# Kernel tuning notes

Hardware: AMD Instinct MI355X
Metric: run time of the kernel (lower is better)

The kernel has to match this reference:

```python
import jax, jax.numpy as jnp
import numpy as np
from jax import lax

BN_EPS = 1e-5

def _maxpool_same(x, k):
    # x: [B, C, H, W]; stride-1 max pool with 'same' padding (pad value -inf, like torch)
    p = k // 2
    neg_inf = jnp.array(-jnp.inf, dtype=x.dtype)
    return lax.reduce_window(x, neg_inf, lax.max,
                             window_dimensions=(1, 1, k, k),
                             window_strides=(1, 1, 1, 1),
                             padding=[(0, 0), (0, 0), (p, p), (p, p)])

def setup_inputs() -> dict:
    key = jax.random.key(0)
    k1, k2 = jax.random.split(key)
    B, Cin, Cout, H, W_ = 16, 1024, 512, 32, 32
    x = jax.random.normal(k1, (B, Cin, H, W_), dtype=jnp.float32)
    W = jax.random.normal(k2, (Cout, Cin), dtype=jnp.float32) * (1.0 / np.sqrt(Cin))
    gamma = jnp.ones((Cout,), dtype=jnp.float32)
    beta = jnp.zeros((Cout,), dtype=jnp.float32)
    running_mean = jnp.zeros((Cout,), dtype=jnp.float32)
    running_var = jnp.ones((Cout,), dtype=jnp.float32)
    return {"x": x, "W": W, "gamma": gamma, "beta": beta,
            "running_mean": running_mean, "running_var": running_var}

def reference(x, W, gamma, beta, running_mean, running_var):
    # 1x1 conv (no bias): [B, Cin, H, W] x [Cout, Cin] -> [B, Cout, H, W]
    y = jnp.einsum('bchw,oc->bohw', x, W)
    # BatchNorm (inference form with running stats)
    inv = gamma * lax.rsqrt(running_var + BN_EPS)
    y = y * inv[None, :, None, None] + (beta - running_mean * inv)[None, :, None, None]
    # Mish activation
    y = y * jnp.tanh(jax.nn.softplus(y))
    # Three overlapping stride-1 max pools, concat channel-wise: [m13, m9, m5, y]
    return jnp.concatenate([_maxpool_same(y, 13), _maxpool_same(y, 9),
                            _maxpool_same(y, 5), y], axis=1)
```

## Files before the change

### kernel.cpp

```cpp
#include <hip/hip_runtime.h>
#include <hip/hip_bf16.h>
#include <math.h>

typedef __attribute__((ext_vector_type(4))) float  f32x4;
typedef __attribute__((ext_vector_type(8))) __bf16 bf16x8;
typedef __attribute__((ext_vector_type(4))) __bf16 bf16x4;

#define BN_EPS 1e-5f

__device__ __forceinline__ void gload16(const void* g, void* l) {
    __builtin_amdgcn_global_load_lds(
        (const __attribute__((address_space(1))) unsigned int*)g,
        (__attribute__((address_space(3))) unsigned int*)l, 16, 0, 0);
}

__global__ __launch_bounds__(256) void prep_transpose_kernel(
    const float* __restrict__ x, __bf16* __restrict__ xt,
    const float* __restrict__ W, const float* __restrict__ gamma,
    const float* __restrict__ beta, const float* __restrict__ rmean,
    const float* __restrict__ rvar, __bf16* __restrict__ Wb,
    float* __restrict__ sc, float* __restrict__ bs)
{
    __shared__ float lt[64][65];
    const int t = threadIdx.x;
    const int bid = blockIdx.x;

    if (bid >= 4096) {
        const int b2 = bid - 4096;
        const int t2 = b2 * 256 + t;
        const int idx = t2 * 4;
        f32x4 v = *(const f32x4*)(W + idx);
        bf16x4 o;
        o[0] = (__bf16)v[0]; o[1] = (__bf16)v[1];
        o[2] = (__bf16)v[2]; o[3] = (__bf16)v[3];
        *(bf16x4*)(Wb + idx) = o;
        if (b2 < 2) {
            int ch = b2 * 256 + t;
            float s = gamma[ch] * rsqrtf(rvar[ch] + BN_EPS);
            sc[ch] = s;
            bs[ch] = beta[ch] - rmean[ch] * s;
        }
        return;
    }

    const int b = bid >> 8;
    const int w = bid & 255;
    const int c0  = (w & 15) * 64;
    const int hw0 = (w >> 4) * 64;

    const int cl = t >> 4;
    const int q  = (t & 15) * 4;
    const float* src = x + (((size_t)(b * 1024 + c0 + cl)) << 10) + hw0 + q;
    #pragma unroll
    for (int i = 0; i < 4; ++i) {
        f32x4 v = *(const f32x4*)(src + ((size_t)i << 14));
        int c = cl + i * 16;
        lt[c][q + 0] = v[0]; lt[c][q + 1] = v[1];
        lt[c][q + 2] = v[2]; lt[c][q + 3] = v[3];
    }
    __syncthreads();

    const int hwl = t >> 3;
    const int oct = (t & 7) * 8;
    #pragma unroll
    for (int half = 0; half < 2; ++half) {
        const int hw = hwl + half * 32;
        bf16x8 v;
        #pragma unroll
        for (int i = 0; i < 8; ++i)
            v[i] = (__bf16)lt[oct + i][hw];
        *(bf16x8*)(xt + (((size_t)(b * 1024 + hw0 + hw)) << 10) + c0 + oct) = v;
    }
}

__global__ __launch_bounds__(256, 4) void gemm_kernel(
    const __bf16* __restrict__ Wb,
    const __bf16* __restrict__ xt,
    const float* __restrict__ sc, const float* __restrict__ bs,
    float* __restrict__ out)
{
    __shared__ __align__(16) char lds[32768];
    char* const Alds = lds;
    char* const Blds = lds + 16384;

    const int t  = threadIdx.x;
    const int f  = blockIdx.x + 4 * (blockIdx.y + 8 * blockIdx.z);
    const int f2 = (f & 7) * 64 + (f >> 3);
    const int o0  = (f2 & 3) * 128;
    const int hw0 = ((f2 >> 2) & 7) * 128;
    const int b   = f2 >> 5;

    const int srow = t >> 3;
    const int sswz = ((t & 7) ^ ((t >> 3) & 7)) * 16;
    const char* Ag = (const char*)Wb + (((size_t)(o0 + srow)) << 11) + sswz;
    const char* Bg = (const char*)xt + ((size_t)b << 21)
                   + (((size_t)(hw0 + srow)) << 11) + sswz;
    char* Al = Alds + t * 16;
    char* Bl = Blds + t * 16;

    const int l  = t & 63;
    const int lr = l & 15;
    const int lk = l >> 4;
    const int wm = (t >> 6) & 1;
    const int wn = t >> 7;

    int aoff[4][2], boff[4][2];
    #pragma unroll
    for (int i = 0; i < 4; ++i)
        #pragma unroll
        for (int kk = 0; kk < 2; ++kk) {
            int ra = wm * 64 + i * 16 + lr;
            int rb = wn * 64 + i * 16 + lr;
            int s  = lk + kk * 4;
            aoff[i][kk] = ra * 128 + ((s ^ (ra & 7)) * 16);
            boff[i][kk] = rb * 128 + ((s ^ (rb & 7)) * 16);
        }

    f32x4 acc[4][4] = {};

    for (int ks = 0; ks < 16; ++ks) {
        __syncthreads();
        const int kb = ks * 128;
        #pragma unroll
        for (int i = 0; i < 4; ++i) {
            gload16(Ag + (i << 16) + kb, Al + (i << 12));
            gload16(Bg + (i << 16) + kb, Bl + (i << 12));
        }
        __syncthreads();
        #pragma unroll
        for (int kk = 0; kk < 2; ++kk) {
            bf16x8 af[4], bfr[4];
            #pragma unroll
            for (int i = 0; i < 4; ++i)
                af[i]  = *(const bf16x8*)(Alds + aoff[i][kk]);
            #pragma unroll
            for (int j = 0; j < 4; ++j)
                bfr[j] = *(const bf16x8*)(Blds + boff[j][kk]);
            #pragma unroll
            for (int i = 0; i < 4; ++i)
                #pragma unroll
                for (int j = 0; j < 4; ++j)
                    acc[i][j] = __builtin_amdgcn_mfma_f32_16x16x32_bf16(
                        af[i], bfr[j], acc[i][j], 0, 0, 0);
        }
    }

    const size_t outbase = (((size_t)b * 2048 + 1536) << 10);
    #pragma unroll
    for (int i = 0; i < 4; ++i) {
        const int ob = o0 + wm * 64 + i * 16 + lk * 4;
        const f32x4 s4 = *(const f32x4*)(sc + ob);
        const f32x4 b4 = *(const f32x4*)(bs + ob);
        #pragma unroll
        for (int r = 0; r < 4; ++r) {
            float* orow = out + outbase + (((size_t)(ob + r)) << 10)
                        + hw0 + wn * 64 + lr;
            #pragma unroll
            for (int j = 0; j < 4; ++j) {
                float v = acc[i][j][r] * s4[r] + b4[r];
                float e   = __expf(fminf(v, 15.0f));
                float num = e * (e + 2.0f);
                orow[j * 16] = v * (num / (num + 2.0f));
            }
        }
    }
}

__global__ __launch_bounds__(256) void pool_kernel(float* __restrict__ out)
{
    __shared__ float A[32][33];
    __shared__ float B[32][33];
    const int t  = threadIdx.x;
    const int id = blockIdx.x;
    const int x8 = id & 7;
    const int j  = id >> 3;
    const int b  = 2 * x8 + (j >> 8);
    const int o2 = (j & 255) * 2;
    const int r  = t >> 3;
    const int c0 = (t & 7) * 4;

    for (int ci = 0; ci < 2; ++ci) {
        const int o = o2 + ci;
        const size_t ybase = ((size_t)(b * 2048 + 1536 + o)) << 10;
        f32x4 v = *(const f32x4*)(out + ybase + t * 4);
        A[r][c0] = v[0]; A[r][c0 + 1] = v[1]; A[r][c0 + 2] = v[2]; A[r][c0 + 3] = v[3];
        __syncthreads();

        for (int p = 0; p < 3; ++p) {
            float wv[8];
            #pragma unroll
            for (int k = 0; k < 8; ++k) {
                int cc = c0 - 2 + k;
                wv[k] = (cc >= 0 && cc < 32) ? A[r][cc] : -INFINITY;
            }
            #pragma unroll
            for (int q = 0; q < 4; ++q) {
                float h = fmaxf(fmaxf(fmaxf(wv[q], wv[q + 1]), fmaxf(wv[q + 2], wv[q + 3])), wv[q + 4]);
                B[r][c0 + q] = h;
            }
            __syncthreads();
            f32x4 m;
            m[0] = m[1] = m[2] = m[3] = -INFINITY;
            #pragma unroll
            for (int k = 0; k < 5; ++k) {
                int rr = r - 2 + k;
                if (rr >= 0 && rr < 32) {
                    m[0] = fmaxf(m[0], B[rr][c0]);
                    m[1] = fmaxf(m[1], B[rr][c0 + 1]);
                    m[2] = fmaxf(m[2], B[rr][c0 + 2]);
                    m[3] = fmaxf(m[3], B[rr][c0 + 3]);
                }
            }
            A[r][c0] = m[0]; A[r][c0 + 1] = m[1]; A[r][c0 + 2] = m[2]; A[r][c0 + 3] = m[3];
            const size_t obase = ((size_t)(b * 2048 + (2 - p) * 512 + o)) << 10;
            *(f32x4*)(out + obase + t * 4) = m;
            __syncthreads();
        }
    }
}

extern "C" void kernel_launch(void* const* d_in, const int* in_sizes, int n_in,
                              void* d_out, int out_size, void* d_ws, size_t ws_size,
                              hipStream_t stream)
{
    const float* x     = (const float*)d_in[0];
    const float* W     = (const float*)d_in[1];
    const float* gamma = (const float*)d_in[2];
    const float* beta  = (const float*)d_in[3];
    const float* rmean = (const float*)d_in[4];
    const float* rvar  = (const float*)d_in[5];
    float* out = (float*)d_out;
    char*  ws  = (char*)d_ws;

    __bf16* xt = (__bf16*)ws;
    __bf16* Wb = (__bf16*)(ws + 33554432);
    float*  sc = (float*)(ws + 34603008);
    float*  bs = (float*)(ws + 34605056);

    prep_transpose_kernel<<<4608, 256, 0, stream>>>(x, xt, W, gamma, beta, rmean, rvar, Wb, sc, bs);
    gemm_kernel<<<dim3(4, 8, 16), 256, 0, stream>>>(Wb, xt, sc, bs, out);
    pool_kernel<<<4096, 256, 0, stream>>>(out);
}
```

Before: 68.65 us.

## Fuse x transpose and bf16 cast into GEMM B-tile loading

Removes the separate transpose kernel that wrote x as a bf16 channel-last copy into workspace. The GEMM now streams fp32 x tiles straight into a larger, swizzled LDS buffer and converts to bf16 while assembling MFMA B fragments. This drops a full read-write pass over the 64MB input. In exchange it doubles LDS bytes per B tile, lowers occupancy to 3 blocks, does scalar LDS reads with conversions in the inner loop, and rereads fp32 x across the 4 output-channel blocks.

```diff
diff --git a/kernel.cpp b/kernel.cpp
--- a/kernel.cpp
+++ b/kernel.cpp
@@ -14,72 +14,33 @@
         (__attribute__((address_space(3))) unsigned int*)l, 16, 0, 0);
 }
 
-__global__ __launch_bounds__(256) void prep_transpose_kernel(
-    const float* __restrict__ x, __bf16* __restrict__ xt,
+__global__ __launch_bounds__(256) void prep_kernel(
     const float* __restrict__ W, const float* __restrict__ gamma,
     const float* __restrict__ beta, const float* __restrict__ rmean,
     const float* __restrict__ rvar, __bf16* __restrict__ Wb,
     float* __restrict__ sc, float* __restrict__ bs)
 {
-    __shared__ float lt[64][65];
-    const int t = threadIdx.x;
-    const int bid = blockIdx.x;
-
-    if (bid >= 4096) {
-        const int b2 = bid - 4096;
-        const int t2 = b2 * 256 + t;
-        const int idx = t2 * 4;
-        f32x4 v = *(const f32x4*)(W + idx);
-        bf16x4 o;
-        o[0] = (__bf16)v[0]; o[1] = (__bf16)v[1];
-        o[2] = (__bf16)v[2]; o[3] = (__bf16)v[3];
-        *(bf16x4*)(Wb + idx) = o;
-        if (b2 < 2) {
-            int ch = b2 * 256 + t;
-            float s = gamma[ch] * rsqrtf(rvar[ch] + BN_EPS);
-            sc[ch] = s;
-            bs[ch] = beta[ch] - rmean[ch] * s;
-        }
-        return;
-    }
-
-    const int b = bid >> 8;
-    const int w = bid & 255;
-    const int c0  = (w & 15) * 64;
-    const int hw0 = (w >> 4) * 64;
-
-    const int cl = t >> 4;
-    const int q  = (t & 15) * 4;
-    const float* src = x + (((size_t)(b * 1024 + c0 + cl)) << 10) + hw0 + q;
-    #pragma unroll
-    for (int i = 0; i < 4; ++i) {
-        f32x4 v = *(const f32x4*)(src + ((size_t)i << 14));
-        int c = cl + i * 16;
-        lt[c][q + 0] = v[0]; lt[c][q + 1] = v[1];
-        lt[c][q + 2] = v[2]; lt[c][q + 3] = v[3];
-    }
-    __syncthreads();
-
-    const int hwl = t >> 3;
-    const int oct = (t & 7) * 8;
-    #pragma unroll
-    for (int half = 0; half < 2; ++half) {
-        const int hw = hwl + half * 32;
-        bf16x8 v;
-        #pragma unroll
-        for (int i = 0; i < 8; ++i)
-            v[i] = (__bf16)lt[oct + i][hw];
-        *(bf16x8*)(xt + (((size_t)(b * 1024 + hw0 + hw)) << 10) + c0 + oct) = v;
-    }
-}
-
-__global__ __launch_bounds__(256, 4) void gemm_kernel(
+    int t = blockIdx.x * 256 + threadIdx.x;
+    int idx = t * 4;
+    f32x4 v = *(const f32x4*)(W + idx);
+    bf16x4 o;
+    o[0] = (__bf16)v[0]; o[1] = (__bf16)v[1];
+    o[2] = (__bf16)v[2]; o[3] = (__bf16)v[3];
+    *(bf16x4*)(Wb + idx) = o;
+    if (t < 512) {
+        float s = gamma[t] * rsqrtf(rvar[t] + BN_EPS);
+        sc[t] = s;
+        bs[t] = beta[t] - rmean[t] * s;
+    }
+}
+
+__global__ __launch_bounds__(256, 3) void gemm_kernel(
     const __bf16* __restrict__ Wb,
-    const __bf16* __restrict__ xt,
+    const float* __restrict__ x,
     const float* __restrict__ sc, const float* __restrict__ bs,
     float* __restrict__ out)
 {
-    __shared__ __align__(16) char lds[32768];
+    __shared__ __align__(16) char lds[49152];
     char* const Alds = lds;
     char* const Blds = lds + 16384;
 
@@ -93,10 +54,18 @@
     const int srow = t >> 3;
     const int sswz = ((t & 7) ^ ((t >> 3) & 7)) * 16;
     const char* Ag = (const char*)Wb + (((size_t)(o0 + srow)) << 11) + sswz;
-    const char* Bg = (const char*)xt + ((size_t)b << 21)
-                   + (((size_t)(hw0 + srow)) << 11) + sswz;
     char* Al = Alds + t * 16;
+
+    int srcoff[8];
+    #pragma unroll
+    for (int r = 0; r < 8; ++r) {
+        int g = r * 256 + t;
+        int c = g >> 5, sp = g & 31;
+        int s = sp ^ (((c >> 3) & 3) << 2);
+        srcoff[r] = c * 1024 + s * 4;
+    }
     char* Bl = Blds + t * 16;
+    const float* xb = x + ((size_t)b << 20) + hw0;
 
     const int l  = t & 63;
     const int lr = l & 15;
@@ -104,17 +73,21 @@
     const int wm = (t >> 6) & 1;
     const int wn = t >> 7;
 
-    int aoff[4][2], boff[4][2];
+    int aoff[4][2];
     #pragma unroll
     for (int i = 0; i < 4; ++i)
         #pragma unroll
         for (int kk = 0; kk < 2; ++kk) {
             int ra = wm * 64 + i * 16 + lr;
-            int rb = wn * 64 + i * 16 + lr;
             int s  = lk + kk * 4;
             aoff[i][kk] = ra * 128 + ((s ^ (ra & 7)) * 16);
-            boff[i][kk] = rb * 128 + ((s ^ (rb & 7)) * 16);
-        }
+        }
+    int noff[4];
+    #pragma unroll
+    for (int j = 0; j < 4; ++j) {
+        int n = wn * 64 + j * 16 + lr;
+        noff[j] = ((((n >> 2) ^ ((lk & 3) << 2))) << 4) + ((n & 3) << 2);
+    }
 
     f32x4 acc[4][4] = {};
 
@@ -122,20 +95,34 @@
         __syncthreads();
         const int kb = ks * 128;
         #pragma unroll
-        for (int i = 0; i < 4; ++i) {
+        for (int i = 0; i < 4; ++i)
             gload16(Ag + (i << 16) + kb, Al + (i << 12));
-            gload16(Bg + (i << 16) + kb, Bl + (i << 12));
-        }
+        const float* xk = xb + ks * 65536;
+        #pragma unroll
+        for (int r = 0; r < 8; ++r)
+            gload16(xk + srcoff[r], Bl + (r << 12));
         __syncthreads();
+
         #pragma unroll
         for (int kk = 0; kk < 2; ++kk) {
             bf16x8 af[4], bfr[4];
             #pragma unroll
             for (int i = 0; i < 4; ++i)
-                af[i]  = *(const bf16x8*)(Alds + aoff[i][kk]);
-            #pragma unroll
-            for (int j = 0; j < 4; ++j)
-                bfr[j] = *(const bf16x8*)(Blds + boff[j][kk]);
+                af[i] = *(const bf16x8*)(Alds + aoff[i][kk]);
+            #pragma unroll
+            for (int j = 0; j < 4; ++j) {
+                const char* pb = Blds + (kk << 14) + (lk << 12) + noff[j];
+                bf16x8 ffr;
+                #pragma unroll
+                for (int p = 0; p < 4; ++p) {
+                    const float* pf = (const float*)(pb + (p << 10));
+                    float f0 = pf[0];
+                    float f1 = pf[128];
+                    ffr[2 * p]     = (__bf16)f0;
+                    ffr[2 * p + 1] = (__bf16)f1;
+                }
+                bfr[j] = ffr;
+            }
             #pragma unroll
             for (int i = 0; i < 4; ++i)
                 #pragma unroll
@@ -232,12 +219,11 @@
     float* out = (float*)d_out;
     char*  ws  = (char*)d_ws;
 
-    __bf16* xt = (__bf16*)ws;
-    __bf16* Wb = (__bf16*)(ws + 33554432);
-    float*  sc = (float*)(ws + 34603008);
-    float*  bs = (float*)(ws + 34605056);
-
-    prep_transpose_kernel<<<4608, 256, 0, stream>>>(x, xt, W, gamma, beta, rmean, rvar, Wb, sc, bs);
-    gemm_kernel<<<dim3(4, 8, 16), 256, 0, stream>>>(Wb, xt, sc, bs, out);
+    __bf16* Wb = (__bf16*)ws;
+    float*  sc = (float*)(ws + 1048576);
+    float*  bs = (float*)(ws + 1050624);
+
+    prep_kernel<<<512, 256, 0, stream>>>(W, gamma, beta, rmean, rvar, Wb, sc, bs);
+    gemm_kernel<<<dim3(4, 8, 16), 256, 0, stream>>>(Wb, x, sc, bs, out);
     pool_kernel<<<4096, 256, 0, stream>>>(out);
 }
```

After: 64.09 us, median of 3. 6.6% less time.
